# Kernel optimization log

Measured on AMD Instinct MI355X. Metric: run time of the kernel, lower is better.

## Reference

```python
import jax, jax.numpy as jnp
import numpy as np

N, E, IN, H, O = 50000, 800000, 256, 8, 32


def setup_inputs() -> dict:
    key = jax.random.key(0)
    ks = jax.random.split(key, 8)
    feat = jax.random.normal(ks[0], (N, IN), dtype=jnp.float32)
    src = jax.random.randint(ks[1], (E,), 0, N, dtype=jnp.int32)
    dst = jax.random.randint(ks[2], (E,), 0, N, dtype=jnp.int32)
    # Xavier-normal-ish parameter init
    W = jax.random.normal(ks[3], (IN, H * O), dtype=jnp.float32) * (2.0 / (IN + H * O)) ** 0.5
    attn_l = jax.random.normal(ks[4], (H, O), dtype=jnp.float32) * (2.0 / (1 + H * O)) ** 0.5
    attn_r = jax.random.normal(ks[5], (H, O), dtype=jnp.float32) * (2.0 / (1 + H * O)) ** 0.5
    bias = jnp.zeros((H * O,), dtype=jnp.float32)
    return {"feat": feat, "W": W, "attn_l": attn_l, "attn_r": attn_r, "bias": bias, "src": src, "dst": dst}


def reference(feat, W, attn_l, attn_r, bias, src, dst):
    # Linear projection: [N, IN] @ [IN, H*O] -> [N, H, O]
    ft = (feat @ W).reshape(-1, H, O)
    # Additive attention logits per node, per head
    el = jnp.einsum('nho,ho->nh', ft, attn_l)  # [N, H]
    er = jnp.einsum('nho,ho->nh', ft, attn_r)  # [N, H]
    # Edge-wise: e = leaky_relu(el[u] + er[v])
    e = jax.nn.leaky_relu(el[src] + er[dst], negative_slope=0.2)  # [E, H]
    # Segment softmax over incoming edges of each destination node
    emax = jax.ops.segment_max(e, dst, num_segments=N)            # [N, H]
    ee = jnp.exp(e - emax[dst])                                   # [E, H]
    denom = jax.ops.segment_sum(ee, dst, num_segments=N)          # [N, H]
    a = ee / denom[dst]                                           # [E, H]
    # Weighted scatter-sum aggregation: sum_u a_{uv} * ft_u
    msg = ft[src] * a[:, :, None]                                 # [E, H, O]
    rst = jax.ops.segment_sum(msg, dst, num_segments=N)           # [N, H, O]
    rst = rst + bias.reshape(1, H, O)
    return rst
```

## Files before the change

kernel.cpp:

```cpp
#include <hip/hip_runtime.h>

#define N_NODES 50000
#define N_EDGES 800000
#define NPAD    50176
#define SPILL_CAP 8192
#define GEMM_BLOCKS 782
#define BUCKET_BLOCKS 391

typedef __bf16 bf16x8 __attribute__((ext_vector_type(8)));
typedef float  fx4    __attribute__((ext_vector_type(4)));
typedef unsigned short us8 __attribute__((ext_vector_type(8)));

__device__ __forceinline__ float b2f(unsigned short u) {
    return __uint_as_float(((unsigned)u) << 16);
}
__device__ __forceinline__ unsigned short f2b(float f) {
    unsigned x = __float_as_uint(f);
    return (unsigned short)((x + 0x7FFFu + ((x >> 16) & 1u)) >> 16);
}

__global__ __launch_bounds__(256) void prep_w(
    const float* __restrict__ W,
    const float* __restrict__ attn_l, const float* __restrict__ attn_r,
    unsigned short* __restrict__ Wt,
    unsigned short* __restrict__ M2t_hi, unsigned short* __restrict__ M2t_lo,
    int* __restrict__ cursor, int* __restrict__ spill_n) {
    __shared__ float T[64 * 65];
    int b = blockIdx.x, t = threadIdx.x;
    if (b < 16) {
        int bi = b >> 2, bj = b & 3;
        int r = t >> 2, cq = t & 3;
        const float* wp = W + (size_t)(bi * 64 + r) * 256 + bj * 64 + cq * 16;
#pragma unroll
        for (int i = 0; i < 16; ++i) T[r * 65 + cq * 16 + i] = wp[i];
        __syncthreads();
        int n = t >> 2, ks = (t & 3) * 16;
        us8 o0, o1;
#pragma unroll
        for (int i = 0; i < 8; ++i) o0[i] = f2b(T[(ks + i) * 65 + n]);
#pragma unroll
        for (int i = 0; i < 8; ++i) o1[i] = f2b(T[(ks + 8 + i) * 65 + n]);
        unsigned short* op = Wt + (size_t)(bj * 64 + n) * 256 + bi * 64 + ks;
        *reinterpret_cast<us8*>(op) = o0;
        *reinterpret_cast<us8*>(op + 8) = o1;
    } else if (b < 32) {
        int j = b - 16;
        const float* av = (j < 8) ? (attn_l + j * 32) : (attn_r + (j - 8) * 32);
        int c0 = (j & 7) * 32;
        float s = 0.f;
#pragma unroll
        for (int o = 0; o < 32; ++o) s += W[t * 256 + c0 + o] * av[o];
        unsigned short h = f2b(s);
        M2t_hi[j * 256 + t] = h;
        M2t_lo[j * 256 + t] = f2b(s - b2f(h));
    } else {
        cursor[(b - 32) * 256 + t] = 0;
        if (b == 32 && t == 0) *spill_n = 0;
    }
}

__global__ __launch_bounds__(512) void gemm_bucket(
    const float* __restrict__ feat,
    const unsigned short* __restrict__ Wt,
    const unsigned short* __restrict__ M2t_hi,
    const unsigned short* __restrict__ M2t_lo,
    unsigned short* __restrict__ ft,
    float* __restrict__ el, float* __restrict__ er,
    const int* __restrict__ src, const int* __restrict__ dst,
    int* __restrict__ cursor, unsigned short* __restrict__ inedge,
    int* __restrict__ spill_n, int2* __restrict__ spill, int stride) {
    __shared__ unsigned short Alds[64 * 264];
    const int tid = threadIdx.x;

    if (blockIdx.x >= GEMM_BLOCKS) {
        int t = (blockIdx.x - GEMM_BLOCKS) * 512 + tid;
        if (t < N_EDGES / 4) {
            int4 s4 = reinterpret_cast<const int4*>(src)[t];
            int4 d4 = reinterpret_cast<const int4*>(dst)[t];
            int ss[4] = {s4.x, s4.y, s4.z, s4.w};
            int dd[4] = {d4.x, d4.y, d4.z, d4.w};
#pragma unroll
            for (int i = 0; i < 4; ++i) {
                int idx = atomicAdd(&cursor[dd[i]], 1);
                if (idx < stride) {
                    inedge[(size_t)dd[i] * stride + idx] = (unsigned short)ss[i];
                } else {
                    int sp = atomicAdd(spill_n, 1);
                    if (sp < SPILL_CAP) spill[sp] = make_int2(ss[i], dd[i]);
                }
            }
        }
        return;
    }

    const int lane = tid & 63;
    const int wid  = tid >> 6;
    const int quad = lane >> 4, l15 = lane & 15;
    const int mbase = blockIdx.x * 64;
    const int nbase = wid * 32;

    const unsigned short* m2base = nullptr;
    if (wid == 1 || wid == 2) {
        int jrow = ((wid == 2) ? 8 : 0) + (l15 & 7);
        m2base = ((l15 < 8) ? M2t_hi : M2t_lo) + jrow * 256;
    }

    fx4 acc[4][2];
    fx4 acce[4];
#pragma unroll
    for (int i = 0; i < 4; ++i) {
        acce[i] = (fx4)0.0f;
#pragma unroll
        for (int j = 0; j < 2; ++j) acc[i][j] = (fx4)0.0f;
    }

    {
        const int srow = tid >> 3, s8 = tid & 7;
        int grow = mbase + srow;
        grow = grow < N_NODES ? grow : N_NODES - 1;
        const float* sp = feat + (size_t)grow * 256;
        unsigned short* sd = &Alds[srow * 264];
#pragma unroll
        for (int ii = 0; ii < 2; ++ii) {
            int c8 = ii * 16 + s8 * 2;
            float4 f0 = *reinterpret_cast<const float4*>(sp + c8 * 8);
            float4 f1 = *reinterpret_cast<const float4*>(sp + c8 * 8 + 4);
            float4 f2 = *reinterpret_cast<const float4*>(sp + c8 * 8 + 8);
            float4 f3 = *reinterpret_cast<const float4*>(sp + c8 * 8 + 12);
            us8 p0, p1;
            p0[0] = f2b(f0.x); p0[1] = f2b(f0.y); p0[2] = f2b(f0.z); p0[3] = f2b(f0.w);
            p0[4] = f2b(f1.x); p0[5] = f2b(f1.y); p0[6] = f2b(f1.z); p0[7] = f2b(f1.w);
            p1[0] = f2b(f2.x); p1[1] = f2b(f2.y); p1[2] = f2b(f2.z); p1[3] = f2b(f2.w);
            p1[4] = f2b(f3.x); p1[5] = f2b(f3.y); p1[6] = f2b(f3.z); p1[7] = f2b(f3.w);
            *reinterpret_cast<us8*>(sd + c8 * 8) = p0;
            *reinterpret_cast<us8*>(sd + c8 * 8 + 8) = p1;
        }
    }
    __syncthreads();

    for (int k0 = 0; k0 < 256; k0 += 32) {
        const int krow = k0 + quad * 8;
        bf16x8 a[4], b[2];
#pragma unroll
        for (int mt = 0; mt < 4; ++mt)
            a[mt] = *reinterpret_cast<const bf16x8*>(&Alds[(mt * 16 + l15) * 264 + krow]);
#pragma unroll
        for (int nt = 0; nt < 2; ++nt)
            b[nt] = *reinterpret_cast<const bf16x8*>(Wt + (nbase + nt * 16 + l15) * 256 + krow);
#pragma unroll
        for (int mt = 0; mt < 4; ++mt)
#pragma unroll
            for (int nt = 0; nt < 2; ++nt)
                acc[mt][nt] = __builtin_amdgcn_mfma_f32_16x16x32_bf16(
                    a[mt], b[nt], acc[mt][nt], 0, 0, 0);
        if (wid == 1 || wid == 2) {
            bf16x8 bm = *reinterpret_cast<const bf16x8*>(m2base + krow);
#pragma unroll
            for (int mt = 0; mt < 4; ++mt)
                acce[mt] = __builtin_amdgcn_mfma_f32_16x16x32_bf16(a[mt], bm, acce[mt], 0, 0, 0);
        }
    }

    if (wid == 1 || wid == 2) {
        float* dstp = (wid == 1) ? el : er;
#pragma unroll
        for (int mt = 0; mt < 4; ++mt) {
#pragma unroll
            for (int r = 0; r < 4; ++r) {
                int row = mbase + mt * 16 + quad * 4 + r;
                float c = acce[mt][r];
                c += __shfl_xor(c, 8);
                if (row < N_NODES && l15 < 8)
                    dstp[row * 8 + l15] = c;
            }
        }
    }
    __syncthreads();

    unsigned short* bw = &Alds[wid * 512];
#pragma unroll
    for (int mt = 0; mt < 4; ++mt) {
#pragma unroll
        for (int r = 0; r < 4; ++r) {
            int rl = quad * 4 + r;
#pragma unroll
            for (int nt = 0; nt < 2; ++nt)
                bw[rl * 32 + nt * 16 + l15] = f2b(acc[mt][nt][r]);
        }
        {
            int rl = lane >> 2;
            int c8 = lane & 3;
            us8 v = *reinterpret_cast<const us8*>(&bw[rl * 32 + c8 * 8]);
            int grow = mbase + mt * 16 + rl;
            if (grow < N_NODES)
                *reinterpret_cast<us8*>(ft + (size_t)grow * 256 + nbase + c8 * 8) = v;
        }
    }
}

__global__ __launch_bounds__(256) void aggregate(
    const unsigned short* __restrict__ ft,
    const float* __restrict__ el, const float* __restrict__ er,
    const int* __restrict__ cursor,
    const unsigned short* __restrict__ inedge,
    const int* __restrict__ spill_n, const int2* __restrict__ spill,
    const float* __restrict__ bias,
    float* __restrict__ out, int stride) {
    int wid = threadIdx.x >> 6, lane = threadIdx.x & 63;
    int v = blockIdx.x * 4 + wid;
    int deg_t = cursor[v];
    int deg = deg_t < stride ? deg_t : stride;
    int half = lane >> 5, l = lane & 31;
    int h = l >> 2;
    int sh = half * 16;
    float erv = er[v * 8 + h];
    const unsigned short* ip = inedge + (size_t)v * stride;
    const us8* ft8 = reinterpret_cast<const us8*>(ft);

    float a[8] = {0.f, 0.f, 0.f, 0.f, 0.f, 0.f, 0.f, 0.f};
    float s = 0.f;
    int j = 0;
    for (; j + 16 <= deg; j += 16) {
        uint4 q0 = *reinterpret_cast<const uint4*>(ip + j);
        uint4 q1 = *reinterpret_cast<const uint4*>(ip + j + 8);
        int u[8];
        u[0] = (q0.x >> sh) & 0xffff; u[1] = (q0.y >> sh) & 0xffff;
        u[2] = (q0.z >> sh) & 0xffff; u[3] = (q0.w >> sh) & 0xffff;
        u[4] = (q1.x >> sh) & 0xffff; u[5] = (q1.y >> sh) & 0xffff;
        u[6] = (q1.z >> sh) & 0xffff; u[7] = (q1.w >> sh) & 0xffff;
        us8 f[8];
#pragma unroll
        for (int t = 0; t < 8; ++t) f[t] = ft8[(size_t)u[t] * 32 + l];
        float ee[8];
#pragma unroll
        for (int t = 0; t < 8; ++t) ee[t] = el[u[t] * 8 + h];
#pragma unroll
        for (int t = 0; t < 8; ++t) {
            float x = ee[t] + erv;
            x = x > 0.f ? x : 0.2f * x;
            float w = __expf(x);
            s += w;
#pragma unroll
            for (int i = 0; i < 8; ++i) a[i] += w * b2f(f[t][i]);
        }
    }
    for (; j + 8 <= deg; j += 8) {
        uint4 q0 = *reinterpret_cast<const uint4*>(ip + j);
        int u[4];
        u[0] = (q0.x >> sh) & 0xffff; u[1] = (q0.y >> sh) & 0xffff;
        u[2] = (q0.z >> sh) & 0xffff; u[3] = (q0.w >> sh) & 0xffff;
        us8 f[4];
#pragma unroll
        for (int t = 0; t < 4; ++t) f[t] = ft8[(size_t)u[t] * 32 + l];
#pragma unroll
        for (int t = 0; t < 4; ++t) {
            float x = el[u[t] * 8 + h] + erv;
            x = x > 0.f ? x : 0.2f * x;
            float w = __expf(x);
            s += w;
#pragma unroll
            for (int i = 0; i < 8; ++i) a[i] += w * b2f(f[t][i]);
        }
    }
    for (; j + 2 <= deg; j += 2) {
        int u = ip[j + half];
        us8 f = ft8[(size_t)u * 32 + l];
        float x = el[u * 8 + h] + erv;
        x = x > 0.f ? x : 0.2f * x;
        float w = __expf(x);
        s += w;
#pragma unroll
        for (int i = 0; i < 8; ++i) a[i] += w * b2f(f[i]);
    }
    if (j < deg && half == 0) {
        int u = ip[j];
        us8 f = ft8[(size_t)u * 32 + l];
        float x = el[u * 8 + h] + erv;
        x = x > 0.f ? x : 0.2f * x;
        float w = __expf(x);
        s += w;
#pragma unroll
        for (int i = 0; i < 8; ++i) a[i] += w * b2f(f[i]);
    }
    if (deg_t > stride) {
        int sn = *spill_n;
        if (sn > SPILL_CAP) sn = SPILL_CAP;
        for (int t = 0; t < sn; ++t) {
            int2 e = spill[t];
            if (e.y == v && half == 0) {
                int u = e.x;
                us8 f = ft8[(size_t)u * 32 + l];
                float x = el[u * 8 + h] + erv;
                x = x > 0.f ? x : 0.2f * x;
                float w = __expf(x);
                s += w;
#pragma unroll
                for (int i = 0; i < 8; ++i) a[i] += w * b2f(f[i]);
            }
        }
    }
#pragma unroll
    for (int i = 0; i < 8; ++i) a[i] += __shfl_xor(a[i], 32);
    s += __shfl_xor(s, 32);
    float inv = deg_t > 0 ? 1.0f / s : 0.f;

    int fi = l * 2 + half;
    float4 bb = reinterpret_cast<const float4*>(bias)[fi];
    int base = half * 4;
    float4 o;
    o.x = a[base + 0] * inv + bb.x;
    o.y = a[base + 1] * inv + bb.y;
    o.z = a[base + 2] * inv + bb.z;
    o.w = a[base + 3] * inv + bb.w;
    reinterpret_cast<float4*>(out)[(size_t)v * 64 + fi] = o;
}

extern "C" void kernel_launch(void* const* d_in, const int* in_sizes, int n_in,
                              void* d_out, int out_size, void* d_ws, size_t ws_size,
                              hipStream_t stream) {
    const float* feat   = (const float*)d_in[0];
    const float* W      = (const float*)d_in[1];
    const float* attn_l = (const float*)d_in[2];
    const float* attn_r = (const float*)d_in[3];
    const float* bias   = (const float*)d_in[4];
    const int* src = (const int*)d_in[5];
    const int* dst = (const int*)d_in[6];
    float* out = (float*)d_out;

    char* ws = (char*)d_ws;
    unsigned short* Wt     = (unsigned short*)(ws + 0);
    unsigned short* M2t_hi = (unsigned short*)(ws + 131072);
    unsigned short* M2t_lo = (unsigned short*)(ws + 139264);
    unsigned short* ft     = (unsigned short*)(ws + 147456);
    float* el              = (float*)(ws + 25747456);
    float* er              = (float*)(ws + 27347456);
    int* cursor            = (int*)(ws + 28947456);
    int* spill_n           = (int*)(ws + 29148160);
    int2* spill            = (int2*)(ws + 29148224);
    unsigned short* inedge = (unsigned short*)(ws + 29213760);

    size_t avail = ws_size > 29213760ull ? ws_size - 29213760ull : 0;
    int stride = (int)(avail / (2ull * NPAD));
    stride &= ~7;
    if (stride > 64) stride = 64;
    if (stride < 8) stride = 8;

    prep_w<<<228, 256, 0, stream>>>(W, attn_l, attn_r, Wt, M2t_hi, M2t_lo,
                                    cursor, spill_n);
    gemm_bucket<<<GEMM_BLOCKS + BUCKET_BLOCKS, 512, 0, stream>>>(
        feat, Wt, M2t_hi, M2t_lo, ft, el, er,
        src, dst, cursor, inedge, spill_n, spill, stride);
    aggregate<<<12500, 256, 0, stream>>>(ft, el, er, cursor, inedge,
                                         spill_n, spill, bias, out, stride);
}
```

Baseline: 226.1 us.

## Fuse prep, GEMM/bucket, and aggregate into one cooperative persistent kernel

Replaces three kernel launches with a single cooperative kernel that uses grid-wide syncs between the weight prep, the GEMM plus edge-bucketing phase, and the aggregation phase. Blocks loop persistently over GEMM tiles, edge chunks and destination nodes, with the grid sized from an occupancy query. The goal is to remove launch gaps and inter-kernel tail effects. The cost is reduced parallelism: at most 1024 blocks, with aggregation handling 8 nodes per block iteration, which may lower latency hiding in the gather-heavy phase. There is a fallback to the old three-kernel path if the cooperative launch fails.

```diff
diff --git a/kernel.cpp b/kernel.cpp
--- a/kernel.cpp
+++ b/kernel.cpp
@@ -1,9 +1,13 @@
 #include <hip/hip_runtime.h>
+#include <hip/hip_cooperative_groups.h>
+
+namespace cg = cooperative_groups;
 
 #define N_NODES 50000
 #define N_EDGES 800000
 #define NPAD    50176
 #define SPILL_CAP 8192
+#define GEMM_TILES 782
 #define GEMM_BLOCKS 782
 #define BUCKET_BLOCKS 391
 
@@ -18,6 +22,294 @@
     unsigned x = __float_as_uint(f);
     return (unsigned short)((x + 0x7FFFu + ((x >> 16) & 1u)) >> 16);
 }
+
+__global__ __launch_bounds__(512) void fused_all(
+    const float* __restrict__ feat, const float* __restrict__ W,
+    const float* __restrict__ attn_l, const float* __restrict__ attn_r,
+    const float* __restrict__ bias,
+    const int* __restrict__ src, const int* __restrict__ dst,
+    unsigned short* __restrict__ Wt,
+    unsigned short* __restrict__ M2t_hi, unsigned short* __restrict__ M2t_lo,
+    unsigned short* __restrict__ ft,
+    float* __restrict__ el, float* __restrict__ er,
+    int* __restrict__ cursor, int* __restrict__ spill_n,
+    int2* __restrict__ spill, unsigned short* __restrict__ inedge,
+    float* __restrict__ out, int stride) {
+    __shared__ unsigned short Alds[64 * 264];
+    cg::grid_group grid = cg::this_grid();
+    const int tid = threadIdx.x;
+    const int bid = blockIdx.x;
+    const int ngrid = gridDim.x;
+
+    {
+        int idx = bid * 512 + tid;
+        if (idx < 8192) {
+            int n = idx & 255, k0 = (idx >> 8) * 8;
+            us8 o;
+#pragma unroll
+            for (int i = 0; i < 8; ++i) o[i] = f2b(W[(k0 + i) * 256 + n]);
+            *reinterpret_cast<us8*>(Wt + n * 256 + k0) = o;
+        } else if (idx < 12288) {
+            int g2 = idx - 8192;
+            int j = g2 >> 8, k = g2 & 255;
+            const float* av = (j < 8) ? (attn_l + j * 32) : (attn_r + (j - 8) * 32);
+            int c0 = (j & 7) * 32;
+            float s = 0.f;
+#pragma unroll
+            for (int o = 0; o < 32; ++o) s += W[k * 256 + c0 + o] * av[o];
+            unsigned short h = f2b(s);
+            M2t_hi[j * 256 + k] = h;
+            M2t_lo[j * 256 + k] = f2b(s - b2f(h));
+        } else if (idx < 24832) {
+            reinterpret_cast<int4*>(cursor)[idx - 12288] = make_int4(0, 0, 0, 0);
+        } else if (idx == 24832) {
+            *spill_n = 0;
+        }
+    }
+    __threadfence();
+    grid.sync();
+
+    {
+        int nbucket = ngrid / 5; if (nbucket < 1) nbucket = 1;
+        int ngemm = ngrid - nbucket;
+        int tpb = (GEMM_TILES + ngemm - 1) / ngemm;
+        ngemm = (GEMM_TILES + tpb - 1) / tpb;
+        nbucket = ngrid - ngemm;
+
+        if (bid >= ngemm) {
+            for (int t = (bid - ngemm) * 512 + tid; t < N_EDGES / 4;
+                 t += nbucket * 512) {
+                int4 s4 = reinterpret_cast<const int4*>(src)[t];
+                int4 d4 = reinterpret_cast<const int4*>(dst)[t];
+                int ss[4] = {s4.x, s4.y, s4.z, s4.w};
+                int dd[4] = {d4.x, d4.y, d4.z, d4.w};
+#pragma unroll
+                for (int i = 0; i < 4; ++i) {
+                    int idx2 = atomicAdd(&cursor[dd[i]], 1);
+                    if (idx2 < stride) {
+                        inedge[(size_t)dd[i] * stride + idx2] = (unsigned short)ss[i];
+                    } else {
+                        int sp = atomicAdd(spill_n, 1);
+                        if (sp < SPILL_CAP) spill[sp] = make_int2(ss[i], dd[i]);
+                    }
+                }
+            }
+        } else {
+            const int lane = tid & 63;
+            const int wid  = tid >> 6;
+            const int quad = lane >> 4, l15 = lane & 15;
+            const int nbase = wid * 32;
+            const unsigned short* m2base = nullptr;
+            if (wid == 1 || wid == 2) {
+                int jrow = ((wid == 2) ? 8 : 0) + (l15 & 7);
+                m2base = ((l15 < 8) ? M2t_hi : M2t_lo) + jrow * 256;
+            }
+            for (int tile = bid; tile < GEMM_TILES; tile += ngemm) {
+                __syncthreads();
+                const int mbase = tile * 64;
+                fx4 acc[4][2];
+                fx4 acce[4];
+#pragma unroll
+                for (int i = 0; i < 4; ++i) {
+                    acce[i] = (fx4)0.0f;
+#pragma unroll
+                    for (int j = 0; j < 2; ++j) acc[i][j] = (fx4)0.0f;
+                }
+                {
+                    const int srow = tid >> 3, s8 = tid & 7;
+                    int grow = mbase + srow;
+                    grow = grow < N_NODES ? grow : N_NODES - 1;
+                    const float* sp = feat + (size_t)grow * 256;
+                    unsigned short* sd = &Alds[srow * 264];
+#pragma unroll
+                    for (int ii = 0; ii < 2; ++ii) {
+                        int c8 = ii * 16 + s8 * 2;
+                        float4 f0 = *reinterpret_cast<const float4*>(sp + c8 * 8);
+                        float4 f1 = *reinterpret_cast<const float4*>(sp + c8 * 8 + 4);
+                        float4 f2 = *reinterpret_cast<const float4*>(sp + c8 * 8 + 8);
+                        float4 f3 = *reinterpret_cast<const float4*>(sp + c8 * 8 + 12);
+                        us8 p0, p1;
+                        p0[0] = f2b(f0.x); p0[1] = f2b(f0.y); p0[2] = f2b(f0.z); p0[3] = f2b(f0.w);
+                        p0[4] = f2b(f1.x); p0[5] = f2b(f1.y); p0[6] = f2b(f1.z); p0[7] = f2b(f1.w);
+                        p1[0] = f2b(f2.x); p1[1] = f2b(f2.y); p1[2] = f2b(f2.z); p1[3] = f2b(f2.w);
+                        p1[4] = f2b(f3.x); p1[5] = f2b(f3.y); p1[6] = f2b(f3.z); p1[7] = f2b(f3.w);
+                        *reinterpret_cast<us8*>(sd + c8 * 8) = p0;
+                        *reinterpret_cast<us8*>(sd + c8 * 8 + 8) = p1;
+                    }
+                }
+                __syncthreads();
+                for (int k0 = 0; k0 < 256; k0 += 32) {
+                    const int krow = k0 + quad * 8;
+                    bf16x8 a[4], b[2];
+#pragma unroll
+                    for (int mt = 0; mt < 4; ++mt)
+                        a[mt] = *reinterpret_cast<const bf16x8*>(&Alds[(mt * 16 + l15) * 264 + krow]);
+#pragma unroll
+                    for (int nt = 0; nt < 2; ++nt)
+                        b[nt] = *reinterpret_cast<const bf16x8*>(Wt + (nbase + nt * 16 + l15) * 256 + krow);
+#pragma unroll
+                    for (int mt = 0; mt < 4; ++mt)
+#pragma unroll
+                        for (int nt = 0; nt < 2; ++nt)
+                            acc[mt][nt] = __builtin_amdgcn_mfma_f32_16x16x32_bf16(
+                                a[mt], b[nt], acc[mt][nt], 0, 0, 0);
+                    if (wid == 1 || wid == 2) {
+                        bf16x8 bm = *reinterpret_cast<const bf16x8*>(m2base + krow);
+#pragma unroll
+                        for (int mt = 0; mt < 4; ++mt)
+                            acce[mt] = __builtin_amdgcn_mfma_f32_16x16x32_bf16(a[mt], bm, acce[mt], 0, 0, 0);
+                    }
+                }
+                if (wid == 1 || wid == 2) {
+                    float* dstp = (wid == 1) ? el : er;
+#pragma unroll
+                    for (int mt = 0; mt < 4; ++mt) {
+#pragma unroll
+                        for (int r = 0; r < 4; ++r) {
+                            int row = mbase + mt * 16 + quad * 4 + r;
+                            float c = acce[mt][r];
+                            c += __shfl_xor(c, 8);
+                            if (row < N_NODES && l15 < 8)
+                                dstp[row * 8 + l15] = c;
+                        }
+                    }
+                }
+                __syncthreads();
+                unsigned short* bw = &Alds[wid * 512];
+#pragma unroll
+                for (int mt = 0; mt < 4; ++mt) {
+#pragma unroll
+                    for (int r = 0; r < 4; ++r) {
+                        int rl = quad * 4 + r;
+#pragma unroll
+                        for (int nt = 0; nt < 2; ++nt)
+                            bw[rl * 32 + nt * 16 + l15] = f2b(acc[mt][nt][r]);
+                    }
+                    {
+                        int rl = lane >> 2;
+                        int c8 = lane & 3;
+                        us8 v = *reinterpret_cast<const us8*>(&bw[rl * 32 + c8 * 8]);
+                        int grow = mbase + mt * 16 + rl;
+                        if (grow < N_NODES)
+                            *reinterpret_cast<us8*>(ft + (size_t)grow * 256 + nbase + c8 * 8) = v;
+                    }
+                }
+            }
+        }
+    }
+    __threadfence();
+    grid.sync();
+
+    {
+        int wid = tid >> 6, lane = tid & 63;
+        int half = lane >> 5, l = lane & 31;
+        int h = l >> 2;
+        int sh = half * 16;
+        const us8* ft8 = reinterpret_cast<const us8*>(ft);
+        for (int v = bid * 8 + wid; v < N_NODES; v += ngrid * 8) {
+            int deg_t = cursor[v];
+            int deg = deg_t < stride ? deg_t : stride;
+            float erv = er[v * 8 + h];
+            const unsigned short* ip = inedge + (size_t)v * stride;
+            float a[8] = {0.f, 0.f, 0.f, 0.f, 0.f, 0.f, 0.f, 0.f};
+            float s = 0.f;
+            int j = 0;
+            for (; j + 16 <= deg; j += 16) {
+                uint4 q0 = *reinterpret_cast<const uint4*>(ip + j);
+                uint4 q1 = *reinterpret_cast<const uint4*>(ip + j + 8);
+                int u[8];
+                u[0] = (q0.x >> sh) & 0xffff; u[1] = (q0.y >> sh) & 0xffff;
+                u[2] = (q0.z >> sh) & 0xffff; u[3] = (q0.w >> sh) & 0xffff;
+                u[4] = (q1.x >> sh) & 0xffff; u[5] = (q1.y >> sh) & 0xffff;
+                u[6] = (q1.z >> sh) & 0xffff; u[7] = (q1.w >> sh) & 0xffff;
+                us8 f[8];
+#pragma unroll
+                for (int t = 0; t < 8; ++t) f[t] = ft8[(size_t)u[t] * 32 + l];
+                float ee[8];
+#pragma unroll
+                for (int t = 0; t < 8; ++t) ee[t] = el[u[t] * 8 + h];
+#pragma unroll
+                for (int t = 0; t < 8; ++t) {
+                    float x = ee[t] + erv;
+                    x = x > 0.f ? x : 0.2f * x;
+                    float w = __expf(x);
+                    s += w;
+#pragma unroll
+                    for (int i = 0; i < 8; ++i) a[i] += w * b2f(f[t][i]);
+                }
+            }
+            for (; j + 8 <= deg; j += 8) {
+                uint4 q0 = *reinterpret_cast<const uint4*>(ip + j);
+                int u[4];
+                u[0] = (q0.x >> sh) & 0xffff; u[1] = (q0.y >> sh) & 0xffff;
+                u[2] = (q0.z >> sh) & 0xffff; u[3] = (q0.w >> sh) & 0xffff;
+                us8 f[4];
+#pragma unroll
+                for (int t = 0; t < 4; ++t) f[t] = ft8[(size_t)u[t] * 32 + l];
+#pragma unroll
+                for (int t = 0; t < 4; ++t) {
+                    float x = el[u[t] * 8 + h] + erv;
+                    x = x > 0.f ? x : 0.2f * x;
+                    float w = __expf(x);
+                    s += w;
+#pragma unroll
+                    for (int i = 0; i < 8; ++i) a[i] += w * b2f(f[t][i]);
+                }
+            }
+            for (; j + 2 <= deg; j += 2) {
+                int u = ip[j + half];
+                us8 f = ft8[(size_t)u * 32 + l];
+                float x = el[u * 8 + h] + erv;
+                x = x > 0.f ? x : 0.2f * x;
+                float w = __expf(x);
+                s += w;
+#pragma unroll
+                for (int i = 0; i < 8; ++i) a[i] += w * b2f(f[i]);
+            }
+            if (j < deg && half == 0) {
+                int u = ip[j];
+                us8 f = ft8[(size_t)u * 32 + l];
+                float x = el[u * 8 + h] + erv;
+                x = x > 0.f ? x : 0.2f * x;
+                float w = __expf(x);
+                s += w;
+#pragma unroll
+                for (int i = 0; i < 8; ++i) a[i] += w * b2f(f[i]);
+            }
+            if (deg_t > stride) {
+                int sn = *spill_n;
+                if (sn > SPILL_CAP) sn = SPILL_CAP;
+                for (int t = 0; t < sn; ++t) {
+                    int2 e = spill[t];
+                    if (e.y == v && half == 0) {
+                        int u = e.x;
+                        us8 f = ft8[(size_t)u * 32 + l];
+                        float x = el[u * 8 + h] + erv;
+                        x = x > 0.f ? x : 0.2f * x;
+                        float w = __expf(x);
+                        s += w;
+#pragma unroll
+                        for (int i = 0; i < 8; ++i) a[i] += w * b2f(f[i]);
+                    }
+                }
+            }
+#pragma unroll
+            for (int i = 0; i < 8; ++i) a[i] += __shfl_xor(a[i], 32);
+            s += __shfl_xor(s, 32);
+            float inv = deg_t > 0 ? 1.0f / s : 0.f;
+            int fi = l * 2 + half;
+            float4 bb = reinterpret_cast<const float4*>(bias)[fi];
+            int base = half * 4;
+            float4 o;
+            o.x = a[base + 0] * inv + bb.x;
+            o.y = a[base + 1] * inv + bb.y;
+            o.z = a[base + 2] * inv + bb.z;
+            o.w = a[base + 3] * inv + bb.w;
+            reinterpret_cast<float4*>(out)[(size_t)v * 64 + fi] = o;
+        }
+    }
+}
+
 
 __global__ __launch_bounds__(256) void prep_w(
     const float* __restrict__ W,
@@ -71,7 +363,6 @@
     int* __restrict__ spill_n, int2* __restrict__ spill, int stride) {
     __shared__ unsigned short Alds[64 * 264];
     const int tid = threadIdx.x;
-
     if (blockIdx.x >= GEMM_BLOCKS) {
         int t = (blockIdx.x - GEMM_BLOCKS) * 512 + tid;
         if (t < N_EDGES / 4) {
@@ -92,19 +383,16 @@
         }
         return;
     }
-
     const int lane = tid & 63;
     const int wid  = tid >> 6;
     const int quad = lane >> 4, l15 = lane & 15;
     const int mbase = blockIdx.x * 64;
     const int nbase = wid * 32;
-
     const unsigned short* m2base = nullptr;
     if (wid == 1 || wid == 2) {
         int jrow = ((wid == 2) ? 8 : 0) + (l15 & 7);
         m2base = ((l15 < 8) ? M2t_hi : M2t_lo) + jrow * 256;
     }
-
     fx4 acc[4][2];
     fx4 acce[4];
 #pragma unroll
@@ -113,7 +401,6 @@
 #pragma unroll
         for (int j = 0; j < 2; ++j) acc[i][j] = (fx4)0.0f;
     }
-
     {
         const int srow = tid >> 3, s8 = tid & 7;
         int grow = mbase + srow;
@@ -137,7 +424,6 @@
         }
     }
     __syncthreads();
-
     for (int k0 = 0; k0 < 256; k0 += 32) {
         const int krow = k0 + quad * 8;
         bf16x8 a[4], b[2];
@@ -160,7 +446,6 @@
                 acce[mt] = __builtin_amdgcn_mfma_f32_16x16x32_bf16(a[mt], bm, acce[mt], 0, 0, 0);
         }
     }
-
     if (wid == 1 || wid == 2) {
         float* dstp = (wid == 1) ? el : er;
 #pragma unroll
@@ -176,7 +461,6 @@
         }
     }
     __syncthreads();
-
     unsigned short* bw = &Alds[wid * 512];
 #pragma unroll
     for (int mt = 0; mt < 4; ++mt) {
@@ -216,7 +500,6 @@
     float erv = er[v * 8 + h];
     const unsigned short* ip = inedge + (size_t)v * stride;
     const us8* ft8 = reinterpret_cast<const us8*>(ft);
-
     float a[8] = {0.f, 0.f, 0.f, 0.f, 0.f, 0.f, 0.f, 0.f};
     float s = 0.f;
     int j = 0;
@@ -303,7 +586,6 @@
     for (int i = 0; i < 8; ++i) a[i] += __shfl_xor(a[i], 32);
     s += __shfl_xor(s, 32);
     float inv = deg_t > 0 ? 1.0f / s : 0.f;
-
     int fi = l * 2 + half;
     float4 bb = reinterpret_cast<const float4*>(bias)[fi];
     int base = half * 4;
@@ -345,11 +627,44 @@
     if (stride > 64) stride = 64;
     if (stride < 8) stride = 8;
 
-    prep_w<<<228, 256, 0, stream>>>(W, attn_l, attn_r, Wt, M2t_hi, M2t_lo,
-                                    cursor, spill_n);
-    gemm_bucket<<<GEMM_BLOCKS + BUCKET_BLOCKS, 512, 0, stream>>>(
-        feat, Wt, M2t_hi, M2t_lo, ft, el, er,
-        src, dst, cursor, inedge, spill_n, spill, stride);
-    aggregate<<<12500, 256, 0, stream>>>(ft, el, er, cursor, inedge,
-                                         spill_n, spill, bias, out, stride);
+    static int coop_grid = -2;
+    if (coop_grid == -2) {
+        int bpc = 0;
+        hipError_t qe = hipOccupancyMaxActiveBlocksPerMultiprocessor(
+            &bpc, fused_all, 512, 0);
+        coop_grid = (qe == hipSuccess && bpc >= 1) ? bpc * 256 : -1;
+        if (coop_grid > 1024) coop_grid = 1024;
+        if (coop_grid >= 0 && coop_grid < 256) coop_grid = -1;
+    }
+
+    bool launched = false;
+    if (coop_grid > 0) {
+        void* kargs[] = {
+            (void*)&feat, (void*)&W, (void*)&attn_l, (void*)&attn_r,
+            (void*)&bias, (void*)&src, (void*)&dst,
+            (void*)&Wt, (void*)&M2t_hi, (void*)&M2t_lo,
+            (void*)&ft, (void*)&el, (void*)&er,
+            (void*)&cursor, (void*)&spill_n, (void*)&spill, (void*)&inedge,
+            (void*)&out, (void*)&stride,
+        };
+        hipError_t le = hipLaunchCooperativeKernel(
+            reinterpret_cast<void*>(fused_all), dim3(coop_grid), dim3(512),
+            kargs, 0, stream);
+        if (le == hipSuccess) {
+            launched = true;
+        } else {
+            (void)hipGetLastError();
+            coop_grid = -1;
+        }
+    }
+
+    if (!launched) {
+        prep_w<<<228, 256, 0, stream>>>(W, attn_l, attn_r, Wt, M2t_hi, M2t_lo,
+                                        cursor, spill_n);
+        gemm_bucket<<<GEMM_BLOCKS + BUCKET_BLOCKS, 512, 0, stream>>>(
+            feat, Wt, M2t_hi, M2t_lo, ft, el, er,
+            src, dst, cursor, inedge, spill_n, spill, stride);
+        aggregate<<<12500, 256, 0, stream>>>(ft, el, er, cursor, inedge,
+                                             spill_n, spill, bias, out, stride);
+    }
 }
```

After: 411.3 us. 81.9% more time.

## Compute attention logits on the fly in aggregate instead of precomputing el/er

Applied to the files above, without the earlier changes.

Removes the precomputed el/er projections (the extra MFMA work in the GEMM and the M2t prep blocks). The aggregate kernel now forms the per-edge logit by dotting the gathered bf16 ft row with attn_l, reduced with two lane shuffles, and computes er from the destination's own ft row. This drops the scattered el gathers and the extra GEMM work, in exchange for more ALU and shuffles per edge and logits computed from bf16-rounded ft. The 8-edge remainder loop is also removed, so those edges now fall through to the 2-edge loop.

```diff
diff --git a/kernel.cpp b/kernel.cpp
--- a/kernel.cpp
+++ b/kernel.cpp
@@ -21,9 +21,7 @@
 
 __global__ __launch_bounds__(256) void prep_w(
     const float* __restrict__ W,
-    const float* __restrict__ attn_l, const float* __restrict__ attn_r,
     unsigned short* __restrict__ Wt,
-    unsigned short* __restrict__ M2t_hi, unsigned short* __restrict__ M2t_lo,
     int* __restrict__ cursor, int* __restrict__ spill_n) {
     __shared__ float T[64 * 65];
     int b = blockIdx.x, t = threadIdx.x;
@@ -43,29 +41,16 @@
         unsigned short* op = Wt + (size_t)(bj * 64 + n) * 256 + bi * 64 + ks;
         *reinterpret_cast<us8*>(op) = o0;
         *reinterpret_cast<us8*>(op + 8) = o1;
-    } else if (b < 32) {
-        int j = b - 16;
-        const float* av = (j < 8) ? (attn_l + j * 32) : (attn_r + (j - 8) * 32);
-        int c0 = (j & 7) * 32;
-        float s = 0.f;
-#pragma unroll
-        for (int o = 0; o < 32; ++o) s += W[t * 256 + c0 + o] * av[o];
-        unsigned short h = f2b(s);
-        M2t_hi[j * 256 + t] = h;
-        M2t_lo[j * 256 + t] = f2b(s - b2f(h));
     } else {
-        cursor[(b - 32) * 256 + t] = 0;
-        if (b == 32 && t == 0) *spill_n = 0;
+        cursor[(b - 16) * 256 + t] = 0;
+        if (b == 16 && t == 0) *spill_n = 0;
     }
 }
 
 __global__ __launch_bounds__(512) void gemm_bucket(
     const float* __restrict__ feat,
     const unsigned short* __restrict__ Wt,
-    const unsigned short* __restrict__ M2t_hi,
-    const unsigned short* __restrict__ M2t_lo,
     unsigned short* __restrict__ ft,
-    float* __restrict__ el, float* __restrict__ er,
     const int* __restrict__ src, const int* __restrict__ dst,
     int* __restrict__ cursor, unsigned short* __restrict__ inedge,
     int* __restrict__ spill_n, int2* __restrict__ spill, int stride) {
@@ -99,20 +84,11 @@
     const int mbase = blockIdx.x * 64;
     const int nbase = wid * 32;
 
-    const unsigned short* m2base = nullptr;
-    if (wid == 1 || wid == 2) {
-        int jrow = ((wid == 2) ? 8 : 0) + (l15 & 7);
-        m2base = ((l15 < 8) ? M2t_hi : M2t_lo) + jrow * 256;
-    }
-
     fx4 acc[4][2];
-    fx4 acce[4];
-#pragma unroll
-    for (int i = 0; i < 4; ++i) {
-        acce[i] = (fx4)0.0f;
+#pragma unroll
+    for (int i = 0; i < 4; ++i)
 #pragma unroll
         for (int j = 0; j < 2; ++j) acc[i][j] = (fx4)0.0f;
-    }
 
     {
         const int srow = tid >> 3, s8 = tid & 7;
@@ -153,27 +129,6 @@
             for (int nt = 0; nt < 2; ++nt)
                 acc[mt][nt] = __builtin_amdgcn_mfma_f32_16x16x32_bf16(
                     a[mt], b[nt], acc[mt][nt], 0, 0, 0);
-        if (wid == 1 || wid == 2) {
-            bf16x8 bm = *reinterpret_cast<const bf16x8*>(m2base + krow);
-#pragma unroll
-            for (int mt = 0; mt < 4; ++mt)
-                acce[mt] = __builtin_amdgcn_mfma_f32_16x16x32_bf16(a[mt], bm, acce[mt], 0, 0, 0);
-        }
-    }
-
-    if (wid == 1 || wid == 2) {
-        float* dstp = (wid == 1) ? el : er;
-#pragma unroll
-        for (int mt = 0; mt < 4; ++mt) {
-#pragma unroll
-            for (int r = 0; r < 4; ++r) {
-                int row = mbase + mt * 16 + quad * 4 + r;
-                float c = acce[mt][r];
-                c += __shfl_xor(c, 8);
-                if (row < N_NODES && l15 < 8)
-                    dstp[row * 8 + l15] = c;
-            }
-        }
     }
     __syncthreads();
 
@@ -200,7 +155,7 @@
 
 __global__ __launch_bounds__(256) void aggregate(
     const unsigned short* __restrict__ ft,
-    const float* __restrict__ el, const float* __restrict__ er,
+    const float* __restrict__ attn_l, const float* __restrict__ attn_r,
     const int* __restrict__ cursor,
     const unsigned short* __restrict__ inedge,
     const int* __restrict__ spill_n, const int2* __restrict__ spill,
@@ -213,9 +168,31 @@
     int half = lane >> 5, l = lane & 31;
     int h = l >> 2;
     int sh = half * 16;
-    float erv = er[v * 8 + h];
     const unsigned short* ip = inedge + (size_t)v * stride;
     const us8* ft8 = reinterpret_cast<const us8*>(ft);
+
+    float al8[8];
+    {
+        const float4* alp = reinterpret_cast<const float4*>(
+            attn_l + h * 32 + (l & 3) * 8);
+        float4 a0 = alp[0], a1 = alp[1];
+        al8[0] = a0.x; al8[1] = a0.y; al8[2] = a0.z; al8[3] = a0.w;
+        al8[4] = a1.x; al8[5] = a1.y; al8[6] = a1.z; al8[7] = a1.w;
+    }
+    float erv;
+    {
+        const float4* arp = reinterpret_cast<const float4*>(
+            attn_r + h * 32 + (l & 3) * 8);
+        float4 r0 = arp[0], r1 = arp[1];
+        us8 fv = ft8[(size_t)v * 32 + l];
+        float d = b2f(fv[0]) * r0.x + b2f(fv[1]) * r0.y +
+                  b2f(fv[2]) * r0.z + b2f(fv[3]) * r0.w +
+                  b2f(fv[4]) * r1.x + b2f(fv[5]) * r1.y +
+                  b2f(fv[6]) * r1.z + b2f(fv[7]) * r1.w;
+        d += __shfl_xor(d, 1);
+        d += __shfl_xor(d, 2);
+        erv = d;
+    }
 
     float a[8] = {0.f, 0.f, 0.f, 0.f, 0.f, 0.f, 0.f, 0.f};
     float s = 0.f;
@@ -231,56 +208,59 @@
         us8 f[8];
 #pragma unroll
         for (int t = 0; t < 8; ++t) f[t] = ft8[(size_t)u[t] * 32 + l];
-        float ee[8];
-#pragma unroll
-        for (int t = 0; t < 8; ++t) ee[t] = el[u[t] * 8 + h];
 #pragma unroll
         for (int t = 0; t < 8; ++t) {
-            float x = ee[t] + erv;
+            float fl[8];
+#pragma unroll
+            for (int i = 0; i < 8; ++i) fl[i] = b2f(f[t][i]);
+            float d = fl[0] * al8[0] + fl[1] * al8[1] + fl[2] * al8[2] +
+                      fl[3] * al8[3] + fl[4] * al8[4] + fl[5] * al8[5] +
+                      fl[6] * al8[6] + fl[7] * al8[7];
+            d += __shfl_xor(d, 1);
+            d += __shfl_xor(d, 2);
+            float x = d + erv;
             x = x > 0.f ? x : 0.2f * x;
             float w = __expf(x);
             s += w;
 #pragma unroll
-            for (int i = 0; i < 8; ++i) a[i] += w * b2f(f[t][i]);
-        }
-    }
-    for (; j + 8 <= deg; j += 8) {
-        uint4 q0 = *reinterpret_cast<const uint4*>(ip + j);
-        int u[4];
-        u[0] = (q0.x >> sh) & 0xffff; u[1] = (q0.y >> sh) & 0xffff;
-        u[2] = (q0.z >> sh) & 0xffff; u[3] = (q0.w >> sh) & 0xffff;
-        us8 f[4];
-#pragma unroll
-        for (int t = 0; t < 4; ++t) f[t] = ft8[(size_t)u[t] * 32 + l];
-#pragma unroll
-        for (int t = 0; t < 4; ++t) {
-            float x = el[u[t] * 8 + h] + erv;
-            x = x > 0.f ? x : 0.2f * x;
-            float w = __expf(x);
-            s += w;
-#pragma unroll
-            for (int i = 0; i < 8; ++i) a[i] += w * b2f(f[t][i]);
+            for (int i = 0; i < 8; ++i) a[i] += w * fl[i];
         }
     }
     for (; j + 2 <= deg; j += 2) {
         int u = ip[j + half];
         us8 f = ft8[(size_t)u * 32 + l];
-        float x = el[u * 8 + h] + erv;
+        float fl[8];
+#pragma unroll
+        for (int i = 0; i < 8; ++i) fl[i] = b2f(f[i]);
+        float d = fl[0] * al8[0] + fl[1] * al8[1] + fl[2] * al8[2] +
+                  fl[3] * al8[3] + fl[4] * al8[4] + fl[5] * al8[5] +
+                  fl[6] * al8[6] + fl[7] * al8[7];
+        d += __shfl_xor(d, 1);
+        d += __shfl_xor(d, 2);
+        float x = d + erv;
         x = x > 0.f ? x : 0.2f * x;
         float w = __expf(x);
         s += w;
 #pragma unroll
-        for (int i = 0; i < 8; ++i) a[i] += w * b2f(f[i]);
+        for (int i = 0; i < 8; ++i) a[i] += w * fl[i];
     }
     if (j < deg && half == 0) {
         int u = ip[j];
         us8 f = ft8[(size_t)u * 32 + l];
-        float x = el[u * 8 + h] + erv;
+        float fl[8];
+#pragma unroll
+        for (int i = 0; i < 8; ++i) fl[i] = b2f(f[i]);
+        float d = fl[0] * al8[0] + fl[1] * al8[1] + fl[2] * al8[2] +
+                  fl[3] * al8[3] + fl[4] * al8[4] + fl[5] * al8[5] +
+                  fl[6] * al8[6] + fl[7] * al8[7];
+        d += __shfl_xor(d, 1);
+        d += __shfl_xor(d, 2);
+        float x = d + erv;
         x = x > 0.f ? x : 0.2f * x;
         float w = __expf(x);
         s += w;
 #pragma unroll
-        for (int i = 0; i < 8; ++i) a[i] += w * b2f(f[i]);
+        for (int i = 0; i < 8; ++i) a[i] += w * fl[i];
     }
     if (deg_t > stride) {
         int sn = *spill_n;
@@ -290,12 +270,20 @@
             if (e.y == v && half == 0) {
                 int u = e.x;
                 us8 f = ft8[(size_t)u * 32 + l];
-                float x = el[u * 8 + h] + erv;
+                float fl[8];
+#pragma unroll
+                for (int i = 0; i < 8; ++i) fl[i] = b2f(f[i]);
+                float d = fl[0] * al8[0] + fl[1] * al8[1] + fl[2] * al8[2] +
+                          fl[3] * al8[3] + fl[4] * al8[4] + fl[5] * al8[5] +
+                          fl[6] * al8[6] + fl[7] * al8[7];
+                d += __shfl_xor(d, 1);
+                d += __shfl_xor(d, 2);
+                float x = d + erv;
                 x = x > 0.f ? x : 0.2f * x;
                 float w = __expf(x);
                 s += w;
 #pragma unroll
-                for (int i = 0; i < 8; ++i) a[i] += w * b2f(f[i]);
+                for (int i = 0; i < 8; ++i) a[i] += w * fl[i];
             }
         }
     }
@@ -329,11 +317,7 @@
 
     char* ws = (char*)d_ws;
     unsigned short* Wt     = (unsigned short*)(ws + 0);
-    unsigned short* M2t_hi = (unsigned short*)(ws + 131072);
-    unsigned short* M2t_lo = (unsigned short*)(ws + 139264);
     unsigned short* ft     = (unsigned short*)(ws + 147456);
-    float* el              = (float*)(ws + 25747456);
-    float* er              = (float*)(ws + 27347456);
     int* cursor            = (int*)(ws + 28947456);
     int* spill_n           = (int*)(ws + 29148160);
     int2* spill            = (int2*)(ws + 29148224);
@@ -345,11 +329,9 @@
     if (stride > 64) stride = 64;
     if (stride < 8) stride = 8;
 
-    prep_w<<<228, 256, 0, stream>>>(W, attn_l, attn_r, Wt, M2t_hi, M2t_lo,
-                                    cursor, spill_n);
+    prep_w<<<212, 256, 0, stream>>>(W, Wt, cursor, spill_n);
     gemm_bucket<<<GEMM_BLOCKS + BUCKET_BLOCKS, 512, 0, stream>>>(
-        feat, Wt, M2t_hi, M2t_lo, ft, el, er,
-        src, dst, cursor, inedge, spill_n, spill, stride);
-    aggregate<<<12500, 256, 0, stream>>>(ft, el, er, cursor, inedge,
+        feat, Wt, ft, src, dst, cursor, inedge, spill_n, spill, stride);
+    aggregate<<<12500, 256, 0, stream>>>(ft, attn_l, attn_r, cursor, inedge,
                                          spill_n, spill, bias, out, stride);
 }
```

Result: slower. 240.9 us (+6.5%).
